# Kernel optimization log

Hardware: AMD Instinct MI355X
Metric: run time of the kernel (lower is better)

Reference implementation:

```python
import jax, jax.numpy as jnp
import numpy as np

D = 1152      # model dim
E = 4         # num_experts
HID = 768     # llama FFN hidden: multiple_of*ceil(int(2*1152/3)/256)
NH = 8        # cross-attention heads
TEMP = 2.0    # expert gumbel temperature (eval: no decay)


def _gumbel_softmax(key, logits, temp, hard):
    g = jax.random.gumbel(key, logits.shape, logits.dtype)
    y = jax.nn.softmax((logits + g) / temp, axis=-1)
    if hard:
        oh = jax.nn.one_hot(jnp.argmax(y, axis=-1), logits.shape[-1], dtype=logits.dtype)
        y = oh - jax.lax.stop_gradient(y) + y
    return y


def _mha(x, mem, in_w, in_b, out_w, out_b):
    # torch nn.MultiheadAttention(batch_first=True): packed qkv in_proj.
    B, S, Dm = x.shape
    hd = Dm // NH
    q = x @ in_w[:Dm].T + in_b[:Dm]
    k = mem @ in_w[Dm:2 * Dm].T + in_b[Dm:2 * Dm]
    v = mem @ in_w[2 * Dm:].T + in_b[2 * Dm:]
    q = q.reshape(B, S, NH, hd).transpose(0, 2, 1, 3)
    k = k.reshape(B, -1, NH, hd).transpose(0, 2, 1, 3)
    v = v.reshape(B, -1, NH, hd).transpose(0, 2, 1, 3)
    a = jax.nn.softmax(jnp.einsum('bhqd,bhkd->bhqk', q, k) / jnp.sqrt(jnp.asarray(hd, x.dtype)), axis=-1)
    o = jnp.einsum('bhqk,bhkd->bhqd', a, v).transpose(0, 2, 1, 3).reshape(B, S, Dm)
    return o @ out_w.T + out_b


def _ff_all(x2d, w1, w2, w3):
    # all E llama SwiGLU experts densely: x2d [N,D], w1/w3 [E,HID,D], w2 [E,D,HID] -> [N,E,D]
    h1 = jnp.einsum('nd,ehd->neh', x2d, w1)
    h3 = jnp.einsum('nd,ehd->neh', x2d, w3)
    return jnp.einsum('neh,edh->ned', jax.nn.silu(h1) * h3, w2)


def setup_inputs() -> dict:
    key = jax.random.key(0)
    ks = jax.random.split(key, 32)
    s = 0.02
    B, S, Sc = 2, 1024, 128
    inp = {
        'x': jax.random.normal(ks[0], (B, S, D), jnp.float32),
        'time': jax.random.normal(ks[1], (B, D), jnp.float32),
        'caption': jax.random.normal(ks[2], (B, Sc, D), jnp.float32),
        'acoustic': jax.random.normal(ks[3], (B, S, D), jnp.float32),
        'attn_in_w': jax.random.normal(ks[4], (3 * D, D), jnp.float32) * s,
        'attn_in_b': jnp.zeros((3 * D,), jnp.float32),
        'attn_out_w': jax.random.normal(ks[5], (D, D), jnp.float32) * s,
        'attn_out_b': jnp.zeros((D,), jnp.float32),
        'hl_w': jax.random.normal(ks[6], (2, D), jnp.float32) * s,
        'hl_b': jnp.zeros((2,), jnp.float32),
        'cap_gate_w': jax.random.normal(ks[7], (E, D), jnp.float32) * s,
        'cap_gate_b': jnp.zeros((E,), jnp.float32),
        'ac_gate_w': jax.random.normal(ks[8], (E, D), jnp.float32) * s,
        'ac_gate_b': jnp.zeros((E,), jnp.float32),
        'cap_w1': jax.random.normal(ks[9], (E, HID, D), jnp.float32) * s,
        'cap_w2': jax.random.normal(ks[10], (E, D, HID), jnp.float32) * s,
        'cap_w3': jax.random.normal(ks[11], (E, HID, D), jnp.float32) * s,
        'ac_w1': jax.random.normal(ks[12], (E, HID, D), jnp.float32) * s,
        'ac_w2': jax.random.normal(ks[13], (E, D, HID), jnp.float32) * s,
        'ac_w3': jax.random.normal(ks[14], (E, HID, D), jnp.float32) * s,
        'fr_w1': jax.random.normal(ks[15], (E, HID, D), jnp.float32) * s,
        'fr_w2': jax.random.normal(ks[16], (E, D, HID), jnp.float32) * s,
        'fr_w3': jax.random.normal(ks[17], (E, HID, D), jnp.float32) * s,
    }
    return inp


def reference(x, time, caption, acoustic,
              attn_in_w, attn_in_b, attn_out_w, attn_out_b,
              hl_w, hl_b, cap_gate_w, cap_gate_b, ac_gate_w, ac_gate_b,
              cap_w1, cap_w2, cap_w3, ac_w1, ac_w2, ac_w3,
              fr_w1, fr_w2, fr_w3):
    B, S, Dm = x.shape
    # cross-attention: x attends over caption, output replaces caption stream
    ca = _mha(x, caption, attn_in_w, attn_in_b, attn_out_w, attn_out_b)
    cap2 = ca.reshape(-1, Dm)          # [N, D]
    x2 = x.reshape(-1, Dm)             # [N, D]
    ac2 = acoustic.reshape(-1, Dm)     # [N, D]
    # high-level caption/acoustic gate from time embedding, broadcast over tokens
    hl = jnp.repeat(time @ hl_w.T + hl_b, S, axis=0)  # [N, 2]
    k1, k2, k3 = jax.random.split(jax.random.key(42), 3)
    hp = _gumbel_softmax(k1, hl, 1.0, False)
    cm = hp[:, 0:1]   # caption mask [N,1]
    am = hp[:, 1:2]   # acoustic mask [N,1]
    # expert gates (eval: hard one-hot straight-through)
    cp = _gumbel_softmax(k2, cap2 @ cap_gate_w.T + cap_gate_b, TEMP, True)  # [N,E]
    ap = _gumbel_softmax(k3, ac2 @ ac_gate_w.T + ac_gate_b, TEMP, True)    # [N,E]
    # dense per-expert SwiGLU, masked combine
    zc = jnp.einsum('ned,ne->nd', _ff_all(x2, cap_w1, cap_w2, cap_w3), cp) * cm
    za = jnp.einsum('ned,ne->nd', _ff_all(x2, ac_w1, ac_w2, ac_w3), ap) * am
    y = (zc + za).reshape(B, S, Dm)
    # frequency experts: each expert sees y masked to its channel block, keeps its block
    r = Dm // E
    region = ((jnp.arange(Dm)[None, :] // r) == jnp.arange(E)[:, None]).astype(x.dtype)  # [E,D]
    ym = y[None] * region[:, None, None, :]  # [E,B,S,D]
    h1 = jnp.einsum('ebsd,ehd->ebsh', ym, fr_w1)
    h3 = jnp.einsum('ebsd,ehd->ebsh', ym, fr_w3)
    fo = jnp.einsum('ebsh,edh->ebsd', jax.nn.silu(h1) * h3, fr_w2)  # [E,B,S,D]
    z = jnp.concatenate([fo[e, :, :, e * r:(e + 1) * r] for e in range(E)], axis=-1)
    # load balancing loss
    probs = jnp.concatenate([cp, ap], axis=1)                                  # [N,2E]
    masks = jnp.concatenate([jnp.tile(cm, (1, E)), jnp.tile(am, (1, E))], axis=1)
    usage = (probs * masks).sum(axis=0) / (masks.sum() + 1e-10)
    lb_loss = jnp.mean(usage * jnp.log(usage + 1e-10))
    return z, lb_loss
```

## Files before the change

### kernel.cpp

```cpp
#include <hip/hip_runtime.h>
#include <stdint.h>

#define NDIM 1152
#define NEXP 4
#define NHID 768
#define NHEAD 8
#define HDIM 144
#define NB 2
#define NS 1024
#define NSC 128
#define NTOK 2048
#define NCAP 256

typedef _Float16 f16;
typedef _Float16 f16x4 __attribute__((ext_vector_type(4)));
typedef _Float16 f16x8 __attribute__((ext_vector_type(8)));
typedef float f32x4 __attribute__((ext_vector_type(4)));

#define MFMA16(a, b, c) __builtin_amdgcn_mfma_f32_16x16x32_f16(a, b, c, 0, 0, 0)

#define WSZ ((size_t)NEXP * NHID * NDIM)
#define WCH ((size_t)(WSZ / 8))

__device__ inline uint2 tfry(uint32_t k0, uint32_t k1, uint32_t x0, uint32_t x1) {
  uint32_t k2 = k0 ^ k1 ^ 0x1BD11BDAu;
#define RND(r) { x0 += x1; x1 = (x1 << r) | (x1 >> (32 - r)); x1 ^= x0; }
  x0 += k0; x1 += k1;
  RND(13) RND(15) RND(26) RND(6)
  x0 += k1; x1 += k2 + 1u;
  RND(17) RND(29) RND(16) RND(24)
  x0 += k2; x1 += k0 + 2u;
  RND(13) RND(15) RND(26) RND(6)
  x0 += k0; x1 += k1 + 3u;
  RND(17) RND(29) RND(16) RND(24)
  x0 += k1; x1 += k2 + 4u;
  RND(13) RND(15) RND(26) RND(6)
  x0 += k2; x1 += k0 + 5u;
#undef RND
  return make_uint2(x0, x1);
}

__device__ inline float b2g(uint32_t bits) {
  uint32_t fb = (bits >> 9) | 0x3f800000u;
  float f = __uint_as_float(fb) - 1.0f;
  const float tiny = 1.1754943508222875e-38f;
  float u = f * 1.0f + tiny;
  u = fmaxf(tiny, u);
  return -logf(-logf(u));
}

__global__ void k_prep(const float* __restrict__ timep, const float* __restrict__ hlw,
                       const float* __restrict__ hlb,
                       float* __restrict__ g1, float* __restrict__ g2, float* __restrict__ g3,
                       float* __restrict__ tl) {
  int t = threadIdx.x;
  uint2 k1 = tfry(0u, 42u, 0u, 0u);
  uint2 k2 = tfry(0u, 42u, 0u, 1u);
  uint2 k3 = tfry(0u, 42u, 0u, 2u);
  for (int p = t; p < 4096; p += 256) {
    uint2 o = tfry(k1.x, k1.y, 0u, (uint32_t)p);
    g1[p] = b2g(o.x ^ o.y);
  }
  for (int p = t; p < 8192; p += 256) {
    uint2 o2 = tfry(k2.x, k2.y, 0u, (uint32_t)p);
    g2[p] = b2g(o2.x ^ o2.y);
    uint2 o3 = tfry(k3.x, k3.y, 0u, (uint32_t)p);
    g3[p] = b2g(o3.x ^ o3.y);
  }
  int wv = t >> 6, lane = t & 63;
  {
    int b = wv >> 1, j = wv & 1;
    float s = 0.f;
    for (int k = lane; k < NDIM; k += 64) s += timep[b * NDIM + k] * hlw[j * NDIM + k];
    for (int m = 32; m; m >>= 1) s += __shfl_xor(s, m);
    if (lane == 0) tl[b * 2 + j] = s + hlb[j];
  }
}

__global__ void k_fuse_gate1(const float* __restrict__ ow, const float* __restrict__ gw,
                             float* __restrict__ wpp) {
  int kt = blockIdx.x % 5;
  int dc = blockIdx.x / 5;
  int k = kt * 256 + threadIdx.x;
  if (k >= NDIM) return;
  float a0 = 0.f, a1 = 0.f, a2 = 0.f, a3 = 0.f;
#pragma unroll 8
  for (int j = 0; j < 64; ++j) {
    int d = dc * 64 + j;
    float o = ow[(size_t)d * NDIM + k];
    a0 += gw[d] * o;
    a1 += gw[NDIM + d] * o;
    a2 += gw[2 * NDIM + d] * o;
    a3 += gw[3 * NDIM + d] * o;
  }
  float* p = wpp + (size_t)dc * 4 * NDIM;
  p[k] = a0; p[NDIM + k] = a1; p[2 * NDIM + k] = a2; p[3 * NDIM + k] = a3;
}

__global__ void k_fuse_gate2(const float* __restrict__ wpp,
                             const float* __restrict__ gw, const float* __restrict__ ob,
                             const float* __restrict__ gb,
                             float* __restrict__ wp, float* __restrict__ bp) {
  if (blockIdx.x == 18) {
    int wv = threadIdx.x >> 6, lane = threadIdx.x & 63;
    float s = 0.f;
    for (int d = lane; d < NDIM; d += 64) s += ob[d] * gw[wv * NDIM + d];
    for (int m = 32; m; m >>= 1) s += __shfl_xor(s, m);
    if (lane == 0) bp[wv] = s + gb[wv];
    return;
  }
  int i = blockIdx.x * 256 + threadIdx.x;
  float s = 0.f;
#pragma unroll
  for (int c = 0; c < 18; ++c) s += wpp[(size_t)c * 4 * NDIM + i];
  wp[i] = s;
}

__global__ void k_ac_logits(const float* __restrict__ ac, const float* __restrict__ agw,
                            const float* __restrict__ agb, float* __restrict__ al) {
  int wv = threadIdx.x >> 6, lane = threadIdx.x & 63;
  int n = blockIdx.x * 4 + wv;
  float s[NEXP] = {0.f, 0.f, 0.f, 0.f};
  for (int d = lane; d < NDIM; d += 64) {
    float a = ac[(size_t)n * NDIM + d];
#pragma unroll
    for (int e = 0; e < NEXP; ++e) s[e] += a * agw[e * NDIM + d];
  }
#pragma unroll
  for (int e = 0; e < NEXP; ++e)
    for (int m = 32; m; m >>= 1) s[e] += __shfl_xor(s[e], m);
  if (lane == 0) {
#pragma unroll
    for (int e = 0; e < NEXP; ++e) al[n * NEXP + e] = s[e] + agb[e];
  }
}

__global__ void k_o_logits(const f16* __restrict__ ohi, const f16* __restrict__ olo,
                           const float* __restrict__ wp, const float* __restrict__ bp,
                           float* __restrict__ cl) {
  int wv = threadIdx.x >> 6, lane = threadIdx.x & 63;
  int n = blockIdx.x * 4 + wv;
  float s[NEXP] = {0.f, 0.f, 0.f, 0.f};
  for (int d = lane; d < NDIM; d += 64) {
    size_t gi = (size_t)n * NDIM + d;
    float a = (float)ohi[gi] + (float)olo[gi] * (1.f / 2048.f);
#pragma unroll
    for (int e = 0; e < NEXP; ++e) s[e] += a * wp[e * NDIM + d];
  }
#pragma unroll
  for (int e = 0; e < NEXP; ++e)
    for (int m = 32; m; m >>= 1) s[e] += __shfl_xor(s[e], m);
  if (lane == 0) {
#pragma unroll
    for (int e = 0; e < NEXP; ++e) cl[n * NEXP + e] = s[e] + bp[e];
  }
}

__global__ void k_cvt_add(const float* __restrict__ srca, const float* __restrict__ srcb,
                          f16* __restrict__ dst, int n) {
  int i = (blockIdx.x * 256 + threadIdx.x) * 4;
  if (i + 3 < n) {
    float4 va = *(const float4*)(srca + i);
    float4 vb = *(const float4*)(srcb + i);
    f16x4 h;
    h[0] = (f16)(va.x + vb.x); h[1] = (f16)(va.y + vb.y);
    h[2] = (f16)(va.z + vb.z); h[3] = (f16)(va.w + vb.w);
    *(f16x4*)(dst + i) = h;
  }
}

__global__ void k_cvt_split(const float* __restrict__ src, f16* __restrict__ hi,
                            f16* __restrict__ lo, int n) {
  int i = (blockIdx.x * 256 + threadIdx.x) * 4;
  if (i + 3 < n) {
    float4 v = *(const float4*)(src + i);
    f16x4 h, l;
    h[0] = (f16)v.x; l[0] = (f16)((v.x - (float)h[0]) * 2048.f);
    h[1] = (f16)v.y; l[1] = (f16)((v.y - (float)h[1]) * 2048.f);
    h[2] = (f16)v.z; l[2] = (f16)((v.z - (float)h[2]) * 2048.f);
    h[3] = (f16)v.w; l[3] = (f16)((v.w - (float)h[3]) * 2048.f);
    *(f16x4*)(hi + i) = h;
    *(f16x4*)(lo + i) = l;
  }
}

__global__ __launch_bounds__(256) void k_gemm_qkv(
    const f16* __restrict__ xhi, const f16* __restrict__ xlo,
    const f16* __restrict__ caphi, const f16* __restrict__ caplo,
    const float* __restrict__ inw, const float* __restrict__ inb,
    f16* __restrict__ qhi, f16* __restrict__ qlo,
    f16* __restrict__ khi, f16* __restrict__ klo,
    f16* __restrict__ vthi, f16* __restrict__ vtlo,
    const float* __restrict__ w0, const float* __restrict__ w1,
    const float* __restrict__ w2, const float* __restrict__ w3,
    f16* __restrict__ wf16) {
  int z = blockIdx.z;
  if (z >= 3) {
    int cvtid = (z - 3) * 576 + blockIdx.y * 18 + blockIdx.x;
    size_t c0 = (size_t)cvtid * 1536;
    int slot = (int)(c0 / WCH);
    size_t base = (c0 % WCH) * 8;
    const float* s = ((slot == 0) ? w0 : (slot == 1) ? w1 : (slot == 2) ? w2 : w3) + base;
    f16* dst = wf16 + (size_t)slot * WSZ + base;
#pragma unroll
    for (int i = 0; i < 6; ++i) {
      size_t off = (size_t)(threadIdx.x + i * 256) * 8;
      float4 v0 = *(const float4*)(s + off);
      float4 v1 = *(const float4*)(s + off + 4);
      f16x8 h;
      h[0] = (f16)v0.x; h[1] = (f16)v0.y; h[2] = (f16)v0.z; h[3] = (f16)v0.w;
      h[4] = (f16)v1.x; h[5] = (f16)v1.y; h[6] = (f16)v1.z; h[7] = (f16)v1.w;
      *(f16x8*)(dst + off) = h;
    }
    return;
  }
  int M = (z == 0) ? NTOK : NCAP;
  int mt = blockIdx.y, nt = blockIdx.x;
  if (mt * 64 >= M) return;
  const f16* Ah_g = (z == 0) ? xhi : caphi;
  const f16* Al_g = (z == 0) ? xlo : caplo;
  __shared__ f16 Ash[64 * 72];
  __shared__ f16 Asl[64 * 72];
  __shared__ f16 Bsh[64 * 72];
  __shared__ f16 Bsl[64 * 72];
  int t = threadIdx.x;
  int wv = t >> 6, lane = t & 63, m16 = lane & 15, quad = lane >> 4;
  int r0 = t >> 3, ak = (t & 7) * 8;
  size_t a0o = (size_t)(mt * 64 + r0) * NDIM;
  size_t a1o = (size_t)(mt * 64 + r0 + 32) * NDIM;
  f32x4 zf = {0.f, 0.f, 0.f, 0.f};
  f32x4 ah[2][2] = {{zf, zf}, {zf, zf}};
  f32x4 am[2][2] = {{zf, zf}, {zf, zf}};
  uint4 rah0, rah1, ral0, ral1;
  float4 rbw[4];
  rah0 = *(const uint4*)(Ah_g + a0o + ak);
  rah1 = *(const uint4*)(Ah_g + a1o + ak);
  ral0 = *(const uint4*)(Al_g + a0o + ak);
  ral1 = *(const uint4*)(Al_g + a1o + ak);
#pragma unroll
  for (int uu = 0; uu < 4; ++uu) {
    int u = t + uu * 256;
    int rr = u >> 4, kp = (u & 15) * 4;
    rbw[uu] = *(const float4*)(inw + (size_t)(z * NDIM + nt * 64 + rr) * NDIM + kp);
  }
  for (int kc = 0; kc < NDIM; kc += 64) {
    __syncthreads();
    *(uint4*)&Ash[r0 * 72 + ak] = rah0;
    *(uint4*)&Ash[(r0 + 32) * 72 + ak] = rah1;
    *(uint4*)&Asl[r0 * 72 + ak] = ral0;
    *(uint4*)&Asl[(r0 + 32) * 72 + ak] = ral1;
#pragma unroll
    for (int uu = 0; uu < 4; ++uu) {
      int u = t + uu * 256;
      int rr = u >> 4, kp = (u & 15) * 4;
      f16x4 hb, lb;
      hb[0] = (f16)rbw[uu].x; lb[0] = (f16)((rbw[uu].x - (float)hb[0]) * 2048.f);
      hb[1] = (f16)rbw[uu].y; lb[1] = (f16)((rbw[uu].y - (float)hb[1]) * 2048.f);
      hb[2] = (f16)rbw[uu].z; lb[2] = (f16)((rbw[uu].z - (float)hb[2]) * 2048.f);
      hb[3] = (f16)rbw[uu].w; lb[3] = (f16)((rbw[uu].w - (float)hb[3]) * 2048.f);
      *(f16x4*)&Bsh[rr * 72 + kp] = hb;
      *(f16x4*)&Bsl[rr * 72 + kp] = lb;
    }
    __syncthreads();
    int kn = kc + 64;
    if (kn < NDIM) {
      rah0 = *(const uint4*)(Ah_g + a0o + kn + ak);
      rah1 = *(const uint4*)(Ah_g + a1o + kn + ak);
      ral0 = *(const uint4*)(Al_g + a0o + kn + ak);
      ral1 = *(const uint4*)(Al_g + a1o + kn + ak);
#pragma unroll
      for (int uu = 0; uu < 4; ++uu) {
        int u = t + uu * 256;
        int rr = u >> 4, kp = (u & 15) * 4;
        rbw[uu] = *(const float4*)(inw + (size_t)(z * NDIM + nt * 64 + rr) * NDIM + kn + kp);
      }
    }
#pragma unroll
    for (int ks = 0; ks < 2; ++ks) {
      int aoff = ((wv & 1) * 32 + m16) * 72 + ks * 32 + quad * 8;
      int boff = ((wv >> 1) * 32 + m16) * 72 + ks * 32 + quad * 8;
      f16x8 a0h = *(const f16x8*)&Ash[aoff];
      f16x8 a1h = *(const f16x8*)&Ash[aoff + 16 * 72];
      f16x8 a0l = *(const f16x8*)&Asl[aoff];
      f16x8 a1l = *(const f16x8*)&Asl[aoff + 16 * 72];
// ... 172 lines not shown
    int po = (wv * 16 + m16) * 136 + ks * 32 + quad * 8;
    f16x8 pah = *(const f16x8*)&Ph[po];
    f16x8 pal = *(const f16x8*)&Pl[po];
#pragma unroll
    for (int nb = 0; nb < 9; ++nb) {
      size_t vo = (size_t)(nb * 16 + m16) * NSC + ks * 32 + quad * 8;
      f16x8 bvh = *(const f16x8*)&vbh[vo];
      f16x8 bvl = *(const f16x8*)&vbl[vo];
      oh_[nb] = MFMA16(pah, bvh, oh_[nb]);
      om_[nb] = MFMA16(pah, bvl, om_[nb]);
      om_[nb] = MFMA16(pal, bvh, om_[nb]);
    }
  }
#pragma unroll
  for (int nb = 0; nb < 9; ++nb)
#pragma unroll
    for (int r = 0; r < 4; ++r) {
      int row = mt * 64 + wv * 16 + quad * 4 + r;
      int col = h * HDIM + nb * 16 + m16;
      float v = oh_[nb][r] + om_[nb][r] * (1.f / 2048.f);
      size_t idx = (size_t)(b * NS + row) * NDIM + col;
      f16 hv = (f16)v;
      ohi[idx] = hv;
      olo[idx] = (f16)((v - (float)hv) * 2048.f);
    }
}

__global__ __launch_bounds__(1024) void k_route(
    const float* __restrict__ cl, const float* __restrict__ al,
    const float* __restrict__ g1, const float* __restrict__ g2,
    const float* __restrict__ g3, const float* __restrict__ tl,
    float* __restrict__ cmv, float* __restrict__ amv,
    int* __restrict__ lists, int* __restrict__ counts, float* __restrict__ out_loss) {
  __shared__ int lcnt[8];
  __shared__ float bins[8];
  __shared__ float ssum[2];
  int t = threadIdx.x;
  if (t < 8) { lcnt[t] = 0; bins[t] = 0.f; }
  if (t < 2) ssum[t] = 0.f;
  __syncthreads();
  for (int n = t; n < NTOK; n += 1024) {
    float lc[NEXP];
#pragma unroll
    for (int e = 0; e < NEXP; ++e) lc[e] = cl[n * NEXP + e] + g2[n * 4 + e];
    int ec = 0; float bv = lc[0];
#pragma unroll
    for (int e = 1; e < NEXP; ++e) if (lc[e] > bv) { bv = lc[e]; ec = e; }
    float la[NEXP];
#pragma unroll
    for (int e = 0; e < NEXP; ++e) la[e] = al[n * NEXP + e] + g3[n * 4 + e];
    int ea = 0; float bva = la[0];
#pragma unroll
    for (int e = 1; e < NEXP; ++e) if (la[e] > bva) { bva = la[e]; ea = e; }
    int b = n >> 10;
    float a0 = tl[b * 2 + 0] + g1[n * 2 + 0];
    float a1 = tl[b * 2 + 1] + g1[n * 2 + 1];
    float mx = fmaxf(a0, a1);
    float e0 = expf(a0 - mx), e1 = expf(a1 - mx);
    float cm = e0 / (e0 + e1), am = e1 / (e0 + e1);
    cmv[n] = cm; amv[n] = am;
    int p0 = atomicAdd(&lcnt[ec], 1);
    lists[ec * NTOK + p0] = n;
    int p1 = atomicAdd(&lcnt[4 + ea], 1);
    lists[(4 + ea) * NTOK + p1] = n;
    atomicAdd(&bins[ec], cm);
    atomicAdd(&bins[4 + ea], am);
    atomicAdd(&ssum[0], cm);
    atomicAdd(&ssum[1], am);
  }
  __syncthreads();
  if (t < 8) counts[t] = lcnt[t];
  if (t == 0) {
    float denom = 4.f * (ssum[0] + ssum[1]) + 1e-10f;
    float acc = 0.f;
    for (int j = 0; j < 8; ++j) {
      float u = bins[j] / denom;
      acc += u * logf(u + 1e-10f);
    }
    out_loss[0] = acc / 8.f;
  }
}

__global__ __launch_bounds__(256) void k_gemm1(
    const f16* __restrict__ x16, const f16* __restrict__ y16,
    f16* wf,
    const int* __restrict__ lists, const int* __restrict__ counts,
    f16* __restrict__ tbuf,
    const float* __restrict__ w4, const float* __restrict__ w5,
    const float* __restrict__ w6, const float* __restrict__ w7,
    const float* __restrict__ w8, int gbase, int G) {
  int bid = blockIdx.x;
  int nblk = G * 384;
  if (bid >= nblk) {
    int cvtid = bid - nblk;
    size_t c0 = (size_t)cvtid * 2048;
    int sg = (int)(c0 / WCH);
    size_t base = (c0 % WCH) * 8;
    const float* s = ((sg == 0) ? w4 : (sg == 1) ? w5 : (sg == 2) ? w6
                       : (sg == 3) ? w7 : w8) + base;
    f16* dst = wf + (size_t)(4 + sg) * WSZ + base;
#pragma unroll
    for (int i = 0; i < 8; ++i) {
      size_t off = (size_t)(threadIdx.x + i * 256) * 8;
      float4 v0 = *(const float4*)(s + off);
      float4 v1 = *(const float4*)(s + off + 4);
      f16x8 h;
      h[0] = (f16)v0.x; h[1] = (f16)v0.y; h[2] = (f16)v0.z; h[3] = (f16)v0.w;
      h[4] = (f16)v1.x; h[5] = (f16)v1.y; h[6] = (f16)v1.z; h[7] = (f16)v1.w;
      *(f16x8*)(dst + off) = h;
    }
    return;
  }
  int xcd = bid & 7;
  int local = bid >> 3;
  int ppx = (G * 12) >> 3;
  int pair = xcd * ppx + (local >> 5);
  int mt = local & 31;
  int g = gbase + pair / 12;
  int nt = pair % 12;
  const f16* A; const f16* B1; const f16* B3; f16* tout;
  const int* list = nullptr;
  int cnt, koff, K;
  if (g < 8) {
    int e = g & 3;
    cnt = counts[g];
    list = lists + g * NTOK;
    A = x16; koff = 0; K = NDIM;
    B1 = wf + (size_t)((g < 4) ? 0 : 2) * WSZ + (size_t)e * NHID * NDIM;
    B3 = wf + (size_t)((g < 4) ? 1 : 3) * WSZ + (size_t)e * NHID * NDIM;
    tout = tbuf + (size_t)g * NTOK * NHID;
  } else {
    int e = g - 8;
    cnt = NTOK;
    A = y16; koff = e * 288; K = 288;
    B1 = wf + (size_t)4 * WSZ + (size_t)e * NHID * NDIM + koff;
    B3 = wf + (size_t)5 * WSZ + (size_t)e * NHID * NDIM + koff;
    tout = tbuf + (size_t)e * NTOK * NHID;
  }
  if (mt * 64 >= cnt) return;
  int t = threadIdx.x;
  int wv = t >> 6, lane = t & 63, m16 = lane & 15, quad = lane >> 4;
  int r0 = t >> 3, ak = (t & 7) * 8;
  int m0 = mt * 64 + r0, m1 = m0 + 32;
  int tok0, tok1;
  if (list) { tok0 = list[min(m0, cnt - 1)]; tok1 = list[min(m1, cnt - 1)]; }
  else { tok0 = m0; tok1 = m1; }
  const f16* ar0 = A + (size_t)tok0 * NDIM + koff;
  const f16* ar1 = A + (size_t)tok1 * NDIM + koff;
  const f16* b1r0 = B1 + (size_t)(nt * 64 + r0) * NDIM;
  const f16* b1r1 = B1 + (size_t)(nt * 64 + r0 + 32) * NDIM;
  const f16* b3r0 = B3 + (size_t)(nt * 64 + r0) * NDIM;
  const f16* b3r1 = B3 + (size_t)(nt * 64 + r0 + 32) * NDIM;
  __shared__ f16 As[64 * 72];
  __shared__ f16 Bs1[64 * 72];
  __shared__ f16 Bs2[64 * 72];
  f32x4 zf = {0.f, 0.f, 0.f, 0.f};
  f32x4 ac1[2][2] = {{zf, zf}, {zf, zf}};
  f32x4 ac2[2][2] = {{zf, zf}, {zf, zf}};
  uint4 z4u = make_uint4(0u, 0u, 0u, 0u);
  uint4 ra0, ra1, rb10, rb11, rb30, rb31;
  {
    bool v = (ak < K);
    ra0  = v ? *(const uint4*)(ar0 + ak) : z4u;
    ra1  = v ? *(const uint4*)(ar1 + ak) : z4u;
    rb10 = v ? *(const uint4*)(b1r0 + ak) : z4u;
    rb11 = v ? *(const uint4*)(b1r1 + ak) : z4u;
    rb30 = v ? *(const uint4*)(b3r0 + ak) : z4u;
    rb31 = v ? *(const uint4*)(b3r1 + ak) : z4u;
  }
  for (int kc = 0; kc < K; kc += 64) {
    __syncthreads();
    *(uint4*)&As[r0 * 72 + ak] = ra0;
    *(uint4*)&As[(r0 + 32) * 72 + ak] = ra1;
    *(uint4*)&Bs1[r0 * 72 + ak] = rb10;
    *(uint4*)&Bs1[(r0 + 32) * 72 + ak] = rb11;
    *(uint4*)&Bs2[r0 * 72 + ak] = rb30;
    *(uint4*)&Bs2[(r0 + 32) * 72 + ak] = rb31;
    __syncthreads();
    int kn = kc + 64;
    if (kn < K) {
      bool v = (kn + ak < K);
      ra0  = v ? *(const uint4*)(ar0 + kn + ak) : z4u;
      ra1  = v ? *(const uint4*)(ar1 + kn + ak) : z4u;
      rb10 = v ? *(const uint4*)(b1r0 + kn + ak) : z4u;
      rb11 = v ? *(const uint4*)(b1r1 + kn + ak) : z4u;
      rb30 = v ? *(const uint4*)(b3r0 + kn + ak) : z4u;
      rb31 = v ? *(const uint4*)(b3r1 + kn + ak) : z4u;
    }
#pragma unroll
    for (int ks = 0; ks < 2; ++ks) {
      int aoff = ((wv & 1) * 32 + m16) * 72 + ks * 32 + quad * 8;
      int boff = ((wv >> 1) * 32 + m16) * 72 + ks * 32 + quad * 8;
      f16x8 a0 = *(const f16x8*)&As[aoff];
      f16x8 a1 = *(const f16x8*)&As[aoff + 16 * 72];
      f16x8 b10 = *(const f16x8*)&Bs1[boff];
      f16x8 b11 = *(const f16x8*)&Bs1[boff + 16 * 72];
      f16x8 b30 = *(const f16x8*)&Bs2[boff];
      f16x8 b31 = *(const f16x8*)&Bs2[boff + 16 * 72];
      ac1[0][0] = MFMA16(a0, b10, ac1[0][0]);
      ac1[0][1] = MFMA16(a0, b11, ac1[0][1]);
      ac1[1][0] = MFMA16(a1, b10, ac1[1][0]);
      ac1[1][1] = MFMA16(a1, b11, ac1[1][1]);
      ac2[0][0] = MFMA16(a0, b30, ac2[0][0]);
      ac2[0][1] = MFMA16(a0, b31, ac2[0][1]);
      ac2[1][0] = MFMA16(a1, b30, ac2[1][0]);
      ac2[1][1] = MFMA16(a1, b31, ac2[1][1]);
    }
  }
#pragma unroll
  for (int mi = 0; mi < 2; ++mi)
#pragma unroll
    for (int ni = 0; ni < 2; ++ni)
#pragma unroll
      for (int r = 0; r < 4; ++r) {
        int row = mt * 64 + (wv & 1) * 32 + mi * 16 + quad * 4 + r;
        int col = nt * 64 + (wv >> 1) * 32 + ni * 16 + m16;
        float h1 = ac1[mi][ni][r];
        float h3 = ac2[mi][ni][r];
        float sl = h1 / (1.0f + expf(-h1));
        tout[(size_t)row * NHID + col] = (f16)(sl * h3);
      }
}

__global__ __launch_bounds__(256) void k_gemm2(
    const f16* __restrict__ tbuf, const f16* __restrict__ wf,
    const int* __restrict__ lists, const int* __restrict__ counts,
    const float* __restrict__ cmv, const float* __restrict__ amv,
    float* __restrict__ yc, float* __restrict__ ya) {
  int bid = blockIdx.x;
  int xcd = bid & 7;
  int local = bid >> 3;
  int pair = xcd * 18 + (local >> 5);
  int mt = local & 31;
  int g = pair / 18;
  int nt = pair % 18;
  int e = g & 3;
  int cnt = counts[g];
  if (mt * 64 >= cnt) return;
  const int* list = lists + g * NTOK;
  const f16* A = tbuf + (size_t)g * NTOK * NHID;
  const f16* Bw = wf + (size_t)((g < 4) ? 6 : 7) * WSZ + (size_t)e * NDIM * NHID;
  const float* sc = (g < 4) ? cmv : amv;
  float* y = (g < 4) ? yc : ya;
  int t = threadIdx.x;
  int wv = t >> 6, lane = t & 63, m16 = lane & 15, quad = lane >> 4;
  int r0 = t >> 3, ak = (t & 7) * 8;
  const f16* ar0 = A + (size_t)(mt * 64 + r0) * NHID;
  const f16* ar1 = A + (size_t)(mt * 64 + r0 + 32) * NHID;
  const f16* br0 = Bw + (size_t)(nt * 64 + r0) * NHID;
  const f16* br1 = Bw + (size_t)(nt * 64 + r0 + 32) * NHID;
  __shared__ f16 As[64 * 72];
  __shared__ f16 Bs[64 * 72];
  f32x4 zf = {0.f, 0.f, 0.f, 0.f};
  f32x4 acc[2][2] = {{zf, zf}, {zf, zf}};
  uint4 ra0, ra1, rb0, rb1;
  ra0 = *(const uint4*)(ar0 + ak);
  ra1 = *(const uint4*)(ar1 + ak);
  rb0 = *(const uint4*)(br0 + ak);
  rb1 = *(const uint4*)(br1 + ak);
  for (int kc = 0; kc < NHID; kc += 64) {
    __syncthreads();
    *(uint4*)&As[r0 * 72 + ak] = ra0;
    *(uint4*)&As[(r0 + 32) * 72 + ak] = ra1;
    *(uint4*)&Bs[r0 * 72 + ak] = rb0;
    *(uint4*)&Bs[(r0 + 32) * 72 + ak] = rb1;
    __syncthreads();
    int kn = kc + 64;
    if (kn < NHID) {
      ra0 = *(const uint4*)(ar0 + kn + ak);
      ra1 = *(const uint4*)(ar1 + kn + ak);
      rb0 = *(const uint4*)(br0 + kn + ak);
      rb1 = *(const uint4*)(br1 + kn + ak);
    }
#pragma unroll
    for (int ks = 0; ks < 2; ++ks) {
      int aoff = ((wv & 1) * 32 + m16) * 72 + ks * 32 + quad * 8;
      int boff = ((wv >> 1) * 32 + m16) * 72 + ks * 32 + quad * 8;
      f16x8 a0 = *(const f16x8*)&As[aoff];
      f16x8 a1 = *(const f16x8*)&As[aoff + 16 * 72];
      f16x8 b0 = *(const f16x8*)&Bs[boff];
      f16x8 b1 = *(const f16x8*)&Bs[boff + 16 * 72];
      acc[0][0] = MFMA16(a0, b0, acc[0][0]);
      acc[0][1] = MFMA16(a0, b1, acc[0][1]);
      acc[1][0] = MFMA16(a1, b0, acc[1][0]);
      acc[1][1] = MFMA16(a1, b1, acc[1][1]);
    }
  }
#pragma unroll
  for (int mi = 0; mi < 2; ++mi)
#pragma unroll
    for (int ni = 0; ni < 2; ++ni)
#pragma unroll
      for (int r = 0; r < 4; ++r) {
        int mg = mt * 64 + (wv & 1) * 32 + mi * 16 + quad * 4 + r;
        if (mg < cnt) {
          int tok = list[mg];
          int col = nt * 64 + (wv >> 1) * 32 + ni * 16 + m16;
          float v = acc[mi][ni][r] * sc[tok];
          y[(size_t)tok * NDIM + col] = v;
        }
      }
}

__global__ __launch_bounds__(256) void k_gemm2_fr(
    const f16* __restrict__ tbuf, const f16* __restrict__ wf, float* __restrict__ zz) {
  int e = blockIdx.z;
  int mt = blockIdx.y, nt = blockIdx.x;
  const f16* A = tbuf + (size_t)e * NTOK * NHID;
  const f16* Bw = wf + (size_t)8 * WSZ + (size_t)e * NDIM * NHID;
  int t = threadIdx.x;
  int wv = t >> 6, lane = t & 63, m16 = lane & 15, quad = lane >> 4;
  int r0 = t >> 3, ak = (t & 7) * 8;
  const f16* ar0 = A + (size_t)(mt * 64 + r0) * NHID;
  const f16* ar1 = A + (size_t)(mt * 64 + r0 + 32) * NHID;
  int ne0 = min(nt * 64 + r0, 287), ne1 = min(nt * 64 + r0 + 32, 287);
  const f16* br0 = Bw + (size_t)(e * 288 + ne0) * NHID;
  const f16* br1 = Bw + (size_t)(e * 288 + ne1) * NHID;
  __shared__ f16 As[64 * 72];
  __shared__ f16 Bs[64 * 72];
  f32x4 zf = {0.f, 0.f, 0.f, 0.f};
  f32x4 acc[2][2] = {{zf, zf}, {zf, zf}};
  uint4 ra0, ra1, rb0, rb1;
  ra0 = *(const uint4*)(ar0 + ak);
  ra1 = *(const uint4*)(ar1 + ak);
  rb0 = *(const uint4*)(br0 + ak);
  rb1 = *(const uint4*)(br1 + ak);
  for (int kc = 0; kc < NHID; kc += 64) {
    __syncthreads();
    *(uint4*)&As[r0 * 72 + ak] = ra0;
    *(uint4*)&As[(r0 + 32) * 72 + ak] = ra1;
    *(uint4*)&Bs[r0 * 72 + ak] = rb0;
    *(uint4*)&Bs[(r0 + 32) * 72 + ak] = rb1;
    __syncthreads();
    int kn = kc + 64;
    if (kn < NHID) {
      ra0 = *(const uint4*)(ar0 + kn + ak);
      ra1 = *(const uint4*)(ar1 + kn + ak);
      rb0 = *(const uint4*)(br0 + kn + ak);
      rb1 = *(const uint4*)(br1 + kn + ak);
    }
#pragma unroll
    for (int ks = 0; ks < 2; ++ks) {
      int aoff = ((wv & 1) * 32 + m16) * 72 + ks * 32 + quad * 8;
      int boff = ((wv >> 1) * 32 + m16) * 72 + ks * 32 + quad * 8;
      f16x8 a0 = *(const f16x8*)&As[aoff];
      f16x8 a1 = *(const f16x8*)&As[aoff + 16 * 72];
      f16x8 b0 = *(const f16x8*)&Bs[boff];
      f16x8 b1 = *(const f16x8*)&Bs[boff + 16 * 72];
      acc[0][0] = MFMA16(a0, b0, acc[0][0]);
      acc[0][1] = MFMA16(a0, b1, acc[0][1]);
      acc[1][0] = MFMA16(a1, b0, acc[1][0]);
      acc[1][1] = MFMA16(a1, b1, acc[1][1]);
    }
  }
#pragma unroll
  for (int mi = 0; mi < 2; ++mi)
#pragma unroll
    for (int ni = 0; ni < 2; ++ni)
#pragma unroll
      for (int r = 0; r < 4; ++r) {
        int cg = nt * 64 + (wv >> 1) * 32 + ni * 16 + m16;
        if (cg < 288) {
          int row = mt * 64 + (wv & 1) * 32 + mi * 16 + quad * 4 + r;
          zz[(size_t)row * NDIM + e * 288 + cg] = acc[mi][ni][r];
        }
      }
}

extern "C" void kernel_launch(void* const* d_in, const int* in_sizes, int n_in,
                              void* d_out, int out_size, void* d_ws, size_t ws_size,
                              hipStream_t stream) {
  const float* x          = (const float*)d_in[0];
  const float* timep      = (const float*)d_in[1];
  const float* caption    = (const float*)d_in[2];
  const float* acoustic   = (const float*)d_in[3];
  const float* attn_in_w  = (const float*)d_in[4];
  const float* attn_in_b  = (const float*)d_in[5];
  const float* attn_out_w = (const float*)d_in[6];
  const float* attn_out_b = (const float*)d_in[7];
  const float* hl_w       = (const float*)d_in[8];
  const float* hl_b       = (const float*)d_in[9];
  const float* cap_gate_w = (const float*)d_in[10];
  const float* cap_gate_b = (const float*)d_in[11];
  const float* ac_gate_w  = (const float*)d_in[12];
  const float* ac_gate_b  = (const float*)d_in[13];
  const float* cap_w1     = (const float*)d_in[14];
  const float* cap_w2     = (const float*)d_in[15];
  const float* cap_w3     = (const float*)d_in[16];
  const float* ac_w1      = (const float*)d_in[17];
  const float* ac_w2      = (const float*)d_in[18];
  const float* ac_w3      = (const float*)d_in[19];
  const float* fr_w1      = (const float*)d_in[20];
  const float* fr_w2      = (const float*)d_in[21];
  const float* fr_w3      = (const float*)d_in[22];
  (void)in_sizes; (void)n_in; (void)out_size; (void)ws_size;

  float* zout = (float*)d_out;
  float* loss = zout + (size_t)NTOK * NDIM;

  char* wsb = (char*)d_ws;
  size_t off = 0;
  auto alloc = [&](size_t bytes) -> void* {
    void* p = wsb + off;
    off = (off + bytes + 255) & ~(size_t)255;
    return p;
  };
  float* g1     = (float*)alloc(4096 * 4);
  float* g2     = (float*)alloc(8192 * 4);
  float* g3     = (float*)alloc(8192 * 4);
  float* tl     = (float*)alloc(4 * 4);
  float* al     = (float*)alloc((size_t)NTOK * NEXP * 4);
  float* cl     = (float*)alloc((size_t)NTOK * NEXP * 4);
  float* cmv    = (float*)alloc((size_t)NTOK * 4);
  float* amv    = (float*)alloc((size_t)NTOK * 4);
  int*   lists  = (int*)alloc((size_t)8 * NTOK * 4);
  int*   counts = (int*)alloc(8 * 4);
  float* wp     = (float*)alloc((size_t)NEXP * NDIM * 4);
  float* bp     = (float*)alloc(NEXP * 4);
  float* wpp    = (float*)alloc((size_t)18 * NEXP * NDIM * 4);
  f16*   xhi    = (f16*)alloc((size_t)NTOK * NDIM * 2);
  f16*   wf16   = (f16*)alloc((size_t)9 * WSZ * 2);
  size_t region = off;
  f16*   xlo    = (f16*)alloc((size_t)NTOK * NDIM * 2);
  f16*   caphi  = (f16*)alloc((size_t)NCAP * NDIM * 2);
  f16*   caplo  = (f16*)alloc((size_t)NCAP * NDIM * 2);
  f16*   qhi    = (f16*)alloc((size_t)NTOK * NDIM * 2);
  f16*   qlo    = (f16*)alloc((size_t)NTOK * NDIM * 2);
  f16*   khi    = (f16*)alloc((size_t)NCAP * NDIM * 2);
  f16*   klo    = (f16*)alloc((size_t)NCAP * NDIM * 2);
  f16*   vthi   = (f16*)alloc((size_t)NB * NDIM * NSC * 2);
  f16*   vtlo   = (f16*)alloc((size_t)NB * NDIM * NSC * 2);
  f16*   ohi    = (f16*)alloc((size_t)NTOK * NDIM * 2);
  f16*   olo    = (f16*)alloc((size_t)NTOK * NDIM * 2);
  off = region;
  f16*   tbuf   = (f16*)alloc((size_t)8 * NTOK * NHID * 2);
  float* ybc    = (float*)alloc((size_t)NTOK * NDIM * 4);
  float* yba    = (float*)alloc((size_t)NTOK * NDIM * 4);
  f16*   y16    = (f16*)alloc((size_t)NTOK * NDIM * 2);

  k_prep<<<dim3(1), dim3(256), 0, stream>>>(timep, hl_w, hl_b, g1, g2, g3, tl);
  k_fuse_gate1<<<dim3(90), dim3(256), 0, stream>>>(attn_out_w, cap_gate_w, wpp);
  k_fuse_gate2<<<dim3(19), dim3(256), 0, stream>>>(wpp, cap_gate_w, attn_out_b,
                                                   cap_gate_b, wp, bp);
  k_ac_logits<<<dim3(512), dim3(256), 0, stream>>>(acoustic, ac_gate_w, ac_gate_b, al);
  k_cvt_split<<<dim3(2304), dim3(256), 0, stream>>>(x, xhi, xlo, NTOK * NDIM);
  k_cvt_split<<<dim3(288), dim3(256), 0, stream>>>(caption, caphi, caplo, NCAP * NDIM);
  k_gemm_qkv<<<dim3(18, 32, 5), dim3(256), 0, stream>>>(
      xhi, xlo, caphi, caplo, attn_in_w, attn_in_b,
      qhi, qlo, khi, klo, vthi, vtlo,
      cap_w1, cap_w3, ac_w1, ac_w3, wf16);
  k_attn<<<dim3(16, 16), dim3(256), 0, stream>>>(qhi, qlo, khi, klo, vthi, vtlo, ohi, olo);
  k_o_logits<<<dim3(512), dim3(256), 0, stream>>>(ohi, olo, wp, bp, cl);
  k_route<<<dim3(1), dim3(1024), 0, stream>>>(cl, al, g1, g2, g3, tl,
                                              cmv, amv, lists, counts, loss);
  k_gemm1<<<dim3(4152), dim3(256), 0, stream>>>(xhi, y16, wf16, lists, counts, tbuf,
                                                fr_w1, fr_w3, cap_w2, ac_w2, fr_w2, 0, 8);
  k_gemm2<<<dim3(4608), dim3(256), 0, stream>>>(tbuf, wf16, lists, counts,
                                                cmv, amv, ybc, yba);
  k_cvt_add<<<dim3(2304), dim3(256), 0, stream>>>(ybc, yba, y16, NTOK * NDIM);
  k_gemm1<<<dim3(1536), dim3(256), 0, stream>>>(xhi, y16, wf16, lists, counts, tbuf,
                                                fr_w1, fr_w3, cap_w2, ac_w2, fr_w2, 8, 4);
  k_gemm2_fr<<<dim3(5, 32, 4), dim3(256), 0, stream>>>(tbuf, wf16, zout);
}
```

Before: 448.0 us.

## Convert only the diagonal frequency-expert weight blocks and fuse y add into fr GEMM

The frequency-expert fp32 weights are now converted to fp16 only for each expert's own 288-channel block (packed compactly), rather than converting all of fr_w1/w3/w2. The separate k_cvt_add kernel is removed: a new k_gemm1_fr reads ybc and yba in fp32, adds them and converts to fp16 while loading its A tiles. The routed k_gemm1 loses its K-bound guards and generic path. This cuts weight-conversion traffic and removes one launch and one intermediate buffer, at the cost of more fp32 activation reads inside the fr GEMM.

Measured after the change: 441.4 us. No clear change (-1.5%).

```diff
diff --git a/kernel.cpp b/kernel.cpp
--- a/kernel.cpp
+++ b/kernel.cpp
@@ -20,7 +20,12 @@
 #define MFMA16(a, b, c) __builtin_amdgcn_mfma_f32_16x16x32_f16(a, b, c, 0, 0, 0)
 
 #define WSZ ((size_t)NEXP * NHID * NDIM)
-#define WCH ((size_t)(WSZ / 8))
+#define WQ  ((size_t)(WSZ / 4))
+#define OFF_CW2 ((size_t)4 * WSZ)
+#define OFF_AW2 ((size_t)5 * WSZ)
+#define OFF_FR1 ((size_t)6 * WSZ)
+#define OFF_FR3 ((size_t)6 * WSZ + WQ)
+#define OFF_FR2 ((size_t)6 * WSZ + 2 * WQ)
 
 __device__ inline uint2 tfry(uint32_t k0, uint32_t k1, uint32_t x0, uint32_t x1) {
   uint32_t k2 = k0 ^ k1 ^ 0x1BD11BDAu;
@@ -156,19 +161,6 @@
   }
 }
 
-__global__ void k_cvt_add(const float* __restrict__ srca, const float* __restrict__ srcb,
-                          f16* __restrict__ dst, int n) {
-  int i = (blockIdx.x * 256 + threadIdx.x) * 4;
-  if (i + 3 < n) {
-    float4 va = *(const float4*)(srca + i);
-    float4 vb = *(const float4*)(srcb + i);
-    f16x4 h;
-    h[0] = (f16)(va.x + vb.x); h[1] = (f16)(va.y + vb.y);
-    h[2] = (f16)(va.z + vb.z); h[3] = (f16)(va.w + vb.w);
-    *(f16x4*)(dst + i) = h;
-  }
-}
-
 __global__ void k_cvt_split(const float* __restrict__ src, f16* __restrict__ hi,
                             f16* __restrict__ lo, int n) {
   int i = (blockIdx.x * 256 + threadIdx.x) * 4;
@@ -197,9 +189,9 @@
   int z = blockIdx.z;
   if (z >= 3) {
     int cvtid = (z - 3) * 576 + blockIdx.y * 18 + blockIdx.x;
-    size_t c0 = (size_t)cvtid * 1536;
-    int slot = (int)(c0 / WCH);
-    size_t base = (c0 % WCH) * 8;
+    size_t c0 = (size_t)cvtid * 12288;
+    int slot = (int)(c0 / WSZ);
+    size_t base = c0 % WSZ;
     const float* s = ((slot == 0) ? w0 : (slot == 1) ? w1 : (slot == 2) ? w2 : w3) + base;
     f16* dst = wf16 + (size_t)slot * WSZ + base;
 #pragma unroll
@@ -538,71 +530,80 @@
 }
 
 __global__ __launch_bounds__(256) void k_gemm1(
-    const f16* __restrict__ x16, const f16* __restrict__ y16,
-    f16* wf,
+    const f16* __restrict__ x16, f16* wf,
     const int* __restrict__ lists, const int* __restrict__ counts,
     f16* __restrict__ tbuf,
     const float* __restrict__ w4, const float* __restrict__ w5,
     const float* __restrict__ w6, const float* __restrict__ w7,
-    const float* __restrict__ w8, int gbase, int G) {
+    const float* __restrict__ w8) {
   int bid = blockIdx.x;
-  int nblk = G * 384;
-  if (bid >= nblk) {
-    int cvtid = bid - nblk;
-    size_t c0 = (size_t)cvtid * 2048;
-    int sg = (int)(c0 / WCH);
-    size_t base = (c0 % WCH) * 8;
-    const float* s = ((sg == 0) ? w4 : (sg == 1) ? w5 : (sg == 2) ? w6
-                       : (sg == 3) ? w7 : w8) + base;
-    f16* dst = wf + (size_t)(4 + sg) * WSZ + base;
-#pragma unroll
-    for (int i = 0; i < 8; ++i) {
-      size_t off = (size_t)(threadIdx.x + i * 256) * 8;
-      float4 v0 = *(const float4*)(s + off);
-      float4 v1 = *(const float4*)(s + off + 4);
-      f16x8 h;
-      h[0] = (f16)v0.x; h[1] = (f16)v0.y; h[2] = (f16)v0.z; h[3] = (f16)v0.w;
-      h[4] = (f16)v1.x; h[5] = (f16)v1.y; h[6] = (f16)v1.z; h[7] = (f16)v1.w;
-      *(f16x8*)(dst + off) = h;
+  if (bid >= 3072) {
+    int cvtid = bid - 3072;
+    int t = threadIdx.x;
+    if (cvtid < 432) {
+      int slot = cvtid / 216;
+      size_t base = (size_t)(cvtid % 216) * 16384;
+      const float* s = (slot ? w7 : w6) + base;
+      f16* dst = wf + (slot ? OFF_AW2 : OFF_CW2) + base;
+#pragma unroll
+      for (int i = 0; i < 8; ++i) {
+        size_t off = (size_t)(t + i * 256) * 8;
+        float4 v0 = *(const float4*)(s + off);
+        float4 v1 = *(const float4*)(s + off + 4);
+        f16x8 h;
+        h[0] = (f16)v0.x; h[1] = (f16)v0.y; h[2] = (f16)v0.z; h[3] = (f16)v0.w;
+        h[4] = (f16)v1.x; h[5] = (f16)v1.y; h[6] = (f16)v1.z; h[7] = (f16)v1.w;
+        *(f16x8*)(dst + off) = h;
+      }
+    } else {
+      int fid = cvtid - 432;
+      int which = fid / 54;
+      int base = (fid % 54) * 16384;
+      const float* s = (which == 0) ? w4 : (which == 1) ? w5 : w8;
+      f16* dst = wf + ((which == 0) ? OFF_FR1 : (which == 1) ? OFF_FR3 : OFF_FR2);
+#pragma unroll
+      for (int i = 0; i < 8; ++i) {
+        int i0 = base + i * 2048 + t * 8;
+        int e = i0 / 221184;
+        int rem = i0 - e * 221184;
+        size_t si;
+        if (which < 2) {
+          int hh = rem / 288, j = rem - (rem / 288) * 288;
+          si = (size_t)e * 884736 + (size_t)hh * 1152 + e * 288 + j;
+        } else {
+          int rr = rem / 768, c = rem - (rem / 768) * 768;
+          si = (size_t)e * 884736 + (size_t)(e * 288 + rr) * 768 + c;
+        }
+        float4 v0 = *(const float4*)(s + si);
+        float4 v1 = *(const float4*)(s + si + 4);
+        f16x8 h;
+        h[0] = (f16)v0.x; h[1] = (f16)v0.y; h[2] = (f16)v0.z; h[3] = (f16)v0.w;
+        h[4] = (f16)v1.x; h[5] = (f16)v1.y; h[6] = (f16)v1.z; h[7] = (f16)v1.w;
+        *(f16x8*)(dst + i0) = h;
+      }
     }
     return;
   }
   int xcd = bid & 7;
   int local = bid >> 3;
-  int ppx = (G * 12) >> 3;
-  int pair = xcd * ppx + (local >> 5);
+  int pair = xcd * 12 + (local >> 5);
   int mt = local & 31;
-  int g = gbase + pair / 12;
+  int g = pair / 12;
   int nt = pair % 12;
-  const f16* A; const f16* B1; const f16* B3; f16* tout;
-  const int* list = nullptr;
-  int cnt, koff, K;
-  if (g < 8) {
-    int e = g & 3;
-    cnt = counts[g];
-    list = lists + g * NTOK;
-    A = x16; koff = 0; K = NDIM;
-    B1 = wf + (size_t)((g < 4) ? 0 : 2) * WSZ + (size_t)e * NHID * NDIM;
-    B3 = wf + (size_t)((g < 4) ? 1 : 3) * WSZ + (size_t)e * NHID * NDIM;
-    tout = tbuf + (size_t)g * NTOK * NHID;
-  } else {
-    int e = g - 8;
-    cnt = NTOK;
-    A = y16; koff = e * 288; K = 288;
-    B1 = wf + (size_t)4 * WSZ + (size_t)e * NHID * NDIM + koff;
-    B3 = wf + (size_t)5 * WSZ + (size_t)e * NHID * NDIM + koff;
-    tout = tbuf + (size_t)e * NTOK * NHID;
-  }
+  int e = g & 3;
+  int cnt = counts[g];
   if (mt * 64 >= cnt) return;
+  const int* list = lists + g * NTOK;
+  const f16* B1 = wf + (size_t)((g < 4) ? 0 : 2) * WSZ + (size_t)e * NHID * NDIM;
+  const f16* B3 = wf + (size_t)((g < 4) ? 1 : 3) * WSZ + (size_t)e * NHID * NDIM;
+  f16* tout = tbuf + (size_t)g * NTOK * NHID;
   int t = threadIdx.x;
   int wv = t >> 6, lane = t & 63, m16 = lane & 15, quad = lane >> 4;
   int r0 = t >> 3, ak = (t & 7) * 8;
   int m0 = mt * 64 + r0, m1 = m0 + 32;
-  int tok0, tok1;
-  if (list) { tok0 = list[min(m0, cnt - 1)]; tok1 = list[min(m1, cnt - 1)]; }
-  else { tok0 = m0; tok1 = m1; }
-  const f16* ar0 = A + (size_t)tok0 * NDIM + koff;
-  const f16* ar1 = A + (size_t)tok1 * NDIM + koff;
+  int tok0 = list[min(m0, cnt - 1)], tok1 = list[min(m1, cnt - 1)];
+  const f16* ar0 = x16 + (size_t)tok0 * NDIM;
+  const f16* ar1 = x16 + (size_t)tok1 * NDIM;
   const f16* b1r0 = B1 + (size_t)(nt * 64 + r0) * NDIM;
   const f16* b1r1 = B1 + (size_t)(nt * 64 + r0 + 32) * NDIM;
   const f16* b3r0 = B3 + (size_t)(nt * 64 + r0) * NDIM;
@@ -613,18 +614,14 @@
   f32x4 zf = {0.f, 0.f, 0.f, 0.f};
   f32x4 ac1[2][2] = {{zf, zf}, {zf, zf}};
   f32x4 ac2[2][2] = {{zf, zf}, {zf, zf}};
-  uint4 z4u = make_uint4(0u, 0u, 0u, 0u);
   uint4 ra0, ra1, rb10, rb11, rb30, rb31;
-  {
-    bool v = (ak < K);
-    ra0  = v ? *(const uint4*)(ar0 + ak) : z4u;
-    ra1  = v ? *(const uint4*)(ar1 + ak) : z4u;
-    rb10 = v ? *(const uint4*)(b1r0 + ak) : z4u;
-    rb11 = v ? *(const uint4*)(b1r1 + ak) : z4u;
-    rb30 = v ? *(const uint4*)(b3r0 + ak) : z4u;
-    rb31 = v ? *(const uint4*)(b3r1 + ak) : z4u;
-  }
-  for (int kc = 0; kc < K; kc += 64) {
+  ra0  = *(const uint4*)(ar0 + ak);
+  ra1  = *(const uint4*)(ar1 + ak);
+  rb10 = *(const uint4*)(b1r0 + ak);
+  rb11 = *(const uint4*)(b1r1 + ak);
+  rb30 = *(const uint4*)(b3r0 + ak);
+  rb31 = *(const uint4*)(b3r1 + ak);
+  for (int kc = 0; kc < NDIM; kc += 64) {
     __syncthreads();
     *(uint4*)&As[r0 * 72 + ak] = ra0;
     *(uint4*)&As[(r0 + 32) * 72 + ak] = ra1;
@@ -634,14 +631,13 @@
     *(uint4*)&Bs2[(r0 + 32) * 72 + ak] = rb31;
     __syncthreads();
     int kn = kc + 64;
-    if (kn < K) {
-      bool v = (kn + ak < K);
-      ra0  = v ? *(const uint4*)(ar0 + kn + ak) : z4u;
-      ra1  = v ? *(const uint4*)(ar1 + kn + ak) : z4u;
-      rb10 = v ? *(const uint4*)(b1r0 + kn + ak) : z4u;
-      rb11 = v ? *(const uint4*)(b1r1 + kn + ak) : z4u;
-      rb30 = v ? *(const uint4*)(b3r0 + kn + ak) : z4u;
-      rb31 = v ? *(const uint4*)(b3r1 + kn + ak) : z4u;
+    if (kn < NDIM) {
+      ra0  = *(const uint4*)(ar0 + kn + ak);
+      ra1  = *(const uint4*)(ar1 + kn + ak);
+      rb10 = *(const uint4*)(b1r0 + kn + ak);
+      rb11 = *(const uint4*)(b1r1 + kn + ak);
+      rb30 = *(const uint4*)(b3r0 + kn + ak);
+      rb31 = *(const uint4*)(b3r1 + kn + ak);
     }
 #pragma unroll
     for (int ks = 0; ks < 2; ++ks) {
@@ -678,6 +674,115 @@
       }
 }
 
+__global__ __launch_bounds__(256) void k_gemm1_fr(
+    const float* __restrict__ ybc, const float* __restrict__ yba,
+    const f16* __restrict__ wf, f16* __restrict__ tbuf) {
+  int e = blockIdx.z, mt = blockIdx.y, nt = blockIdx.x;
+  const int K = 288;
+  int koff = e * 288;
+  const f16* B1 = wf + OFF_FR1 + (size_t)e * 768 * 288;
+  const f16* B3 = wf + OFF_FR3 + (size_t)e * 768 * 288;
+  f16* tout = tbuf + (size_t)e * NTOK * NHID;
+  int t = threadIdx.x;
+  int wv = t >> 6, lane = t & 63, m16 = lane & 15, quad = lane >> 4;
+  int r0 = t >> 3, ak = (t & 7) * 8;
+  const float* c0 = ybc + (size_t)(mt * 64 + r0) * NDIM + koff;
+  const float* c1 = ybc + (size_t)(mt * 64 + r0 + 32) * NDIM + koff;
+  const float* d0 = yba + (size_t)(mt * 64 + r0) * NDIM + koff;
+  const float* d1 = yba + (size_t)(mt * 64 + r0 + 32) * NDIM + koff;
+  const f16* b1r0 = B1 + (size_t)(nt * 64 + r0) * 288;
+  const f16* b1r1 = B1 + (size_t)(nt * 64 + r0 + 32) * 288;
+  const f16* b3r0 = B3 + (size_t)(nt * 64 + r0) * 288;
+  const f16* b3r1 = B3 + (size_t)(nt * 64 + r0 + 32) * 288;
+  __shared__ f16 As[64 * 72];
+  __shared__ f16 Bs1[64 * 72];
+  __shared__ f16 Bs2[64 * 72];
+  f32x4 zf = {0.f, 0.f, 0.f, 0.f};
+  f32x4 ac1[2][2] = {{zf, zf}, {zf, zf}};
+  f32x4 ac2[2][2] = {{zf, zf}, {zf, zf}};
+  uint4 rb10, rb11, rb30, rb31;
+  rb10 = *(const uint4*)(b1r0 + ak);
+  rb11 = *(const uint4*)(b1r1 + ak);
+  rb30 = *(const uint4*)(b3r0 + ak);
+  rb31 = *(const uint4*)(b3r1 + ak);
+  for (int kc = 0; kc < K; kc += 64) {
+    __syncthreads();
+    {
+      f16x8 h0, h1;
+      int cb = kc + ak;
+      if (cb < K) {
+        float4 p0 = *(const float4*)(c0 + cb);
+        float4 p1 = *(const float4*)(c0 + cb + 4);
+        float4 q0 = *(const float4*)(d0 + cb);
+        float4 q1 = *(const float4*)(d0 + cb + 4);
+        h0[0] = (f16)(p0.x + q0.x); h0[1] = (f16)(p0.y + q0.y);
+        h0[2] = (f16)(p0.z + q0.z); h0[3] = (f16)(p0.w + q0.w);
+        h0[4] = (f16)(p1.x + q1.x); h0[5] = (f16)(p1.y + q1.y);
+        h0[6] = (f16)(p1.z + q1.z); h0[7] = (f16)(p1.w + q1.w);
+        p0 = *(const float4*)(c1 + cb);
+        p1 = *(const float4*)(c1 + cb + 4);
+        q0 = *(const float4*)(d1 + cb);
+        q1 = *(const float4*)(d1 + cb + 4);
+        h1[0] = (f16)(p0.x + q0.x); h1[1] = (f16)(p0.y + q0.y);
+        h1[2] = (f16)(p0.z + q0.z); h1[3] = (f16)(p0.w + q0.w);
+        h1[4] = (f16)(p1.x + q1.x); h1[5] = (f16)(p1.y + q1.y);
+        h1[6] = (f16)(p1.z + q1.z); h1[7] = (f16)(p1.w + q1.w);
+      } else {
+#pragma unroll
+        for (int j = 0; j < 8; ++j) { h0[j] = (f16)0.f; h1[j] = (f16)0.f; }
+      }
+      *(f16x8*)&As[r0 * 72 + ak] = h0;
+      *(f16x8*)&As[(r0 + 32) * 72 + ak] = h1;
+    }
+    *(uint4*)&Bs1[r0 * 72 + ak] = rb10;
+    *(uint4*)&Bs1[(r0 + 32) * 72 + ak] = rb11;
+    *(uint4*)&Bs2[r0 * 72 + ak] = rb30;
+    *(uint4*)&Bs2[(r0 + 32) * 72 + ak] = rb31;
+    __syncthreads();
+    int kn = kc + 64;
+    if (kn < K) {
+      bool v = (kn + ak < K);
+      uint4 z4u = make_uint4(0u, 0u, 0u, 0u);
+      rb10 = v ? *(const uint4*)(b1r0 + kn + ak) : z4u;
+      rb11 = v ? *(const uint4*)(b1r1 + kn + ak) : z4u;
+      rb30 = v ? *(const uint4*)(b3r0 + kn + ak) : z4u;
+      rb31 = v ? *(const uint4*)(b3r1 + kn + ak) : z4u;
+    }
+#pragma unroll
+    for (int ks = 0; ks < 2; ++ks) {
+      int aoff = ((wv & 1) * 32 + m16) * 72 + ks * 32 + quad * 8;
+      int boff = ((wv >> 1) * 32 + m16) * 72 + ks * 32 + quad * 8;
+      f16x8 a0 = *(const f16x8*)&As[aoff];
+      f16x8 a1 = *(const f16x8*)&As[aoff + 16 * 72];
+      f16x8 b10 = *(const f16x8*)&Bs1[boff];
+      f16x8 b11 = *(const f16x8*)&Bs1[boff + 16 * 72];
+      f16x8 b30 = *(const f16x8*)&Bs2[boff];
+      f16x8 b31 = *(const f16x8*)&Bs2[boff + 16 * 72];
+      ac1[0][0] = MFMA16(a0, b10, ac1[0][0]);
+      ac1[0][1] = MFMA16(a0, b11, ac1[0][1]);
+      ac1[1][0] = MFMA16(a1, b10, ac1[1][0]);
+      ac1[1][1] = MFMA16(a1, b11, ac1[1][1]);
+      ac2[0][0] = MFMA16(a0, b30, ac2[0][0]);
+      ac2[0][1] = MFMA16(a0, b31, ac2[0][1]);
+      ac2[1][0] = MFMA16(a1, b30, ac2[1][0]);
+      ac2[1][1] = MFMA16(a1, b31, ac2[1][1]);
+    }
+  }
+#pragma unroll
+  for (int mi = 0; mi < 2; ++mi)
+#pragma unroll
+    for (int ni = 0; ni < 2; ++ni)
+#pragma unroll
+      for (int r = 0; r < 4; ++r) {
+        int row = mt * 64 + (wv & 1) * 32 + mi * 16 + quad * 4 + r;
+        int col = nt * 64 + (wv >> 1) * 32 + ni * 16 + m16;
+        float h1v = ac1[mi][ni][r];
+        float h3v = ac2[mi][ni][r];
+        float sl = h1v / (1.0f + expf(-h1v));
+        tout[(size_t)row * NHID + col] = (f16)(sl * h3v);
+      }
+}
+
 __global__ __launch_bounds__(256) void k_gemm2(
     const f16* __restrict__ tbuf, const f16* __restrict__ wf,
     const int* __restrict__ lists, const int* __restrict__ counts,
@@ -695,7 +800,7 @@
   if (mt * 64 >= cnt) return;
   const int* list = lists + g * NTOK;
   const f16* A = tbuf + (size_t)g * NTOK * NHID;
-  const f16* Bw = wf + (size_t)((g < 4) ? 6 : 7) * WSZ + (size_t)e * NDIM * NHID;
+  const f16* Bw = wf + ((g < 4) ? OFF_CW2 : OFF_AW2) + (size_t)e * NDIM * NHID;
   const float* sc = (g < 4) ? cmv : amv;
   float* y = (g < 4) ? yc : ya;
   int t = threadIdx.x;
@@ -763,15 +868,15 @@
   int e = blockIdx.z;
   int mt = blockIdx.y, nt = blockIdx.x;
   const f16* A = tbuf + (size_t)e * NTOK * NHID;
-  const f16* Bw = wf + (size_t)8 * WSZ + (size_t)e * NDIM * NHID;
+  const f16* Bw = wf + OFF_FR2 + (size_t)e * 288 * NHID;
   int t = threadIdx.x;
   int wv = t >> 6, lane = t & 63, m16 = lane & 15, quad = lane >> 4;
   int r0 = t >> 3, ak = (t & 7) * 8;
   const f16* ar0 = A + (size_t)(mt * 64 + r0) * NHID;
   const f16* ar1 = A + (size_t)(mt * 64 + r0 + 32) * NHID;
   int ne0 = min(nt * 64 + r0, 287), ne1 = min(nt * 64 + r0 + 32, 287);
-  const f16* br0 = Bw + (size_t)(e * 288 + ne0) * NHID;
-  const f16* br1 = Bw + (size_t)(e * 288 + ne1) * NHID;
+  const f16* br0 = Bw + (size_t)ne0 * NHID;
+  const f16* br1 = Bw + (size_t)ne1 * NHID;
   __shared__ f16 As[64 * 72];
   __shared__ f16 Bs[64 * 72];
   f32x4 zf = {0.f, 0.f, 0.f, 0.f};
@@ -875,7 +980,7 @@
   float* bp     = (float*)alloc(NEXP * 4);
   float* wpp    = (float*)alloc((size_t)18 * NEXP * NDIM * 4);
   f16*   xhi    = (f16*)alloc((size_t)NTOK * NDIM * 2);
-  f16*   wf16   = (f16*)alloc((size_t)9 * WSZ * 2);
+  f16*   wf16   = (f16*)alloc((size_t)(6 * WSZ + 3 * WQ) * 2);
   size_t region = off;
   f16*   xlo    = (f16*)alloc((size_t)NTOK * NDIM * 2);
   f16*   caphi  = (f16*)alloc((size_t)NCAP * NDIM * 2);
@@ -892,7 +997,6 @@
   f16*   tbuf   = (f16*)alloc((size_t)8 * NTOK * NHID * 2);
   float* ybc    = (float*)alloc((size_t)NTOK * NDIM * 4);
   float* yba    = (float*)alloc((size_t)NTOK * NDIM * 4);
-  f16*   y16    = (f16*)alloc((size_t)NTOK * NDIM * 2);
 
   k_prep<<<dim3(1), dim3(256), 0, stream>>>(timep, hl_w, hl_b, g1, g2, g3, tl);
   k_fuse_gate1<<<dim3(90), dim3(256), 0, stream>>>(attn_out_w, cap_gate_w, wpp);
@@ -909,12 +1013,10 @@
   k_o_logits<<<dim3(512), dim3(256), 0, stream>>>(ohi, olo, wp, bp, cl);
   k_route<<<dim3(1), dim3(1024), 0, stream>>>(cl, al, g1, g2, g3, tl,
                                               cmv, amv, lists, counts, loss);
-  k_gemm1<<<dim3(4152), dim3(256), 0, stream>>>(xhi, y16, wf16, lists, counts, tbuf,
-                                                fr_w1, fr_w3, cap_w2, ac_w2, fr_w2, 0, 8);
+  k_gemm1<<<dim3(3666), dim3(256), 0, stream>>>(xhi, wf16, lists, counts, tbuf,
+                                                fr_w1, fr_w3, cap_w2, ac_w2, fr_w2);
   k_gemm2<<<dim3(4608), dim3(256), 0, stream>>>(tbuf, wf16, lists, counts,
                                                 cmv, amv, ybc, yba);
-  k_cvt_add<<<dim3(2304), dim3(256), 0, stream>>>(ybc, yba, y16, NTOK * NDIM);
-  k_gemm1<<<dim3(1536), dim3(256), 0, stream>>>(xhi, y16, wf16, lists, counts, tbuf,
-                                                fr_w1, fr_w3, cap_w2, ac_w2, fr_w2, 8, 4);
+  k_gemm1_fr<<<dim3(12, 32, 4), dim3(256), 0, stream>>>(ybc, yba, wf16, tbuf);
   k_gemm2_fr<<<dim3(5, 32, 4), dim3(256), 0, stream>>>(tbuf, wf16, zout);
 }
```
